# Optimization experiments

Hardware: AMD Instinct MI355X
Metric: run time of the kernel (lower is better)

## Reference

```python
import jax, jax.numpy as jnp
import numpy as np

B, T, C = 2, 2048, 1024
NH = 16
HD = C // NH

def build_alibi_bias(n_head, max_len):
    slopes = jnp.arange(1, n_head + 1, dtype=jnp.float32) / n_head  # [nh]
    ar = jnp.arange(max_len, dtype=jnp.float32)
    # bias[h, i, j] = slopes[h] * (j - i)
    return slopes[:, None, None] * (ar[None, None, :] - ar[None, :, None])

def setup_inputs() -> dict:
    key = jax.random.key(0)
    ks = jax.random.split(key, 7)
    s = 0.02
    return {
        "x": jax.random.normal(ks[0], (B, T, C), dtype=jnp.float32),
        "q_w": jax.random.normal(ks[1], (C, C), dtype=jnp.float32) * s,   # [in, out]
        "q_b": jnp.zeros((C,), dtype=jnp.float32),
        "kv_w": jax.random.normal(ks[2], (C, 2 * C), dtype=jnp.float32) * s,
        "kv_b": jnp.zeros((2 * C,), dtype=jnp.float32),
        "o_w": jax.random.normal(ks[3], (C, C), dtype=jnp.float32) * s,
        "o_b": jnp.zeros((C,), dtype=jnp.float32),
    }

def reference(x, q_w, q_b, kv_w, kv_b, o_w, o_b):
    Bx, Tx, Cx = x.shape
    q = (x @ q_w + q_b).reshape(Bx, Tx, NH, HD).transpose(0, 2, 1, 3)      # [B,nh,T,hd]
    kv = (x @ kv_w + kv_b).reshape(Bx, Tx, 2, NH, HD).transpose(2, 0, 3, 1, 4)
    k, v = kv[0], kv[1]                                                     # [B,nh,T,hd]
    att = jnp.einsum("bhqd,bhkd->bhqk", q, k) * (1.0 / np.sqrt(HD))        # [B,nh,T,T]
    att = att + build_alibi_bias(NH, Tx)[None]                              # ALiBi bias
    causal = jnp.tril(jnp.ones((Tx, Tx), dtype=bool))
    att = jnp.where(causal[None, None], att, -jnp.inf)
    att = jax.nn.softmax(att, axis=-1)
    y = jnp.einsum("bhqk,bhkd->bhqd", att, v)                               # [B,nh,T,hd]
    y = y.transpose(0, 2, 1, 3).reshape(Bx, Tx, Cx)
    return y @ o_w + o_b
```

## Files before the change

### kernel.cpp

```cpp
#include <hip/hip_runtime.h>
#include <hip/hip_bf16.h>

#define NB 2
#define NT 2048
#define NC 1024
#define NHD 16
#define HDD 64
#define LOG2E 1.4426950408889634f

typedef __attribute__((ext_vector_type(8))) short short8;
typedef __attribute__((ext_vector_type(4))) float f32x4;
typedef __attribute__((ext_vector_type(16))) float f32x16;

__device__ __forceinline__ ushort f2bf(float f) {
    union { float f; unsigned u; } v; v.f = f;
    unsigned u = v.u;
    unsigned r = (u + 0x7FFFu + ((u >> 16) & 1u)) >> 16;
    return (ushort)r;
}

__device__ __forceinline__ unsigned pkbf(float a, float b) {
    __hip_bfloat162 t = __float22bfloat162_rn(float2{a, b});
    unsigned u; __builtin_memcpy(&u, &t, 4); return u;
}

__device__ __forceinline__ void gload16(const ushort* g, ushort* l) {
    __builtin_amdgcn_global_load_lds((const __attribute__((address_space(1))) void*)g,
                                     (__attribute__((address_space(3))) void*)l, 16, 0, 0);
}

__device__ __forceinline__ void tcvt_tile(const float* __restrict__ src, ushort* __restrict__ dst,
                                          int Kd, int Nd, int kb, int nb)
{
    __shared__ ushort tile[64][68];
    const int tid = threadIdx.x;
    const int r = tid >> 2, c = (tid & 3) * 16;
    const float* sp = src + (size_t)(kb + r) * Nd + nb + c;
#pragma unroll
    for (int i = 0; i < 16; i += 4) {
        float4 v = *(const float4*)(sp + i);
        tile[r][c + i + 0] = f2bf(v.x);
        tile[r][c + i + 1] = f2bf(v.y);
        tile[r][c + i + 2] = f2bf(v.z);
        tile[r][c + i + 3] = f2bf(v.w);
    }
    __syncthreads();
    ushort* dp = dst + (size_t)(nb + r) * Kd + kb + c;
#pragma unroll
    for (int i = 0; i < 16; i += 8) {
        short8 o;
#pragma unroll
        for (int j = 0; j < 8; j++) o[j] = (short)tile[c + i + j][r];
        *(short8*)(dp + i) = o;
    }
}

__global__ __launch_bounds__(256)
void prep(const float* __restrict__ x, const float* __restrict__ q_w,
          const float* __restrict__ kv_w, const float* __restrict__ o_w,
          ushort* __restrict__ xb, ushort* __restrict__ wqkvT, ushort* __restrict__ woT)
{
    const int bid = blockIdx.x;
    if (bid < 2048) {
        int i = (bid * 256 + threadIdx.x) * 8;
        float4 a = *(const float4*)(x + i);
        float4 b = *(const float4*)(x + i + 4);
        short8 o;
        o[0] = (short)f2bf(a.x); o[1] = (short)f2bf(a.y);
        o[2] = (short)f2bf(a.z); o[3] = (short)f2bf(a.w);
        o[4] = (short)f2bf(b.x); o[5] = (short)f2bf(b.y);
        o[6] = (short)f2bf(b.z); o[7] = (short)f2bf(b.w);
        *(short8*)(xb + i) = o;
    } else if (bid < 2304) {
        int r = bid - 2048;
        tcvt_tile(q_w, wqkvT, 1024, 1024, (r & 15) * 64, (r >> 4) * 64);
    } else if (bid < 2816) {
        int r = bid - 2304;
        tcvt_tile(kv_w, wqkvT + 1024 * 1024, 1024, 2048, (r & 15) * 64, (r >> 4) * 64);
    } else {
        int r = bid - 2816;
        tcvt_tile(o_w, woT, 1024, 1024, (r & 15) * 64, (r >> 4) * 64);
    }
}

__global__ __launch_bounds__(256)
void vtr(const ushort* __restrict__ src, ushort* __restrict__ dst)
{
    __shared__ ushort tile[64][66];
    const int tid = threadIdx.x;
    const int bh = blockIdx.y;
    const int t0 = blockIdx.x * 64;
    const int r = tid >> 2, c = (tid & 3) * 16;
    const ushort* sp = src + ((size_t)bh * NT + t0 + r) * HDD + c;
    *(short8*)&tile[r][c]     = *(const short8*)sp;
    *(short8*)&tile[r][c + 8] = *(const short8*)(sp + 8);
    __syncthreads();
    ushort* dp = dst + ((size_t)bh * HDD + r) * NT + t0 + c;
    short8 o0, o1;
#pragma unroll
    for (int j = 0; j < 8; j++) { o0[j] = (short)tile[c + j][r]; o1[j] = (short)tile[c + 8 + j][r]; }
    *(short8*)dp = o0;
    *(short8*)(dp + 8) = o1;
}

template<int MODE>
__global__ __launch_bounds__(256)
void gemm128(const ushort* __restrict__ A, const ushort* __restrict__ Bt,
             const float* __restrict__ bias0, const float* __restrict__ bias1,
             ushort* __restrict__ Qo, ushort* __restrict__ Ko, ushort* __restrict__ Vo,
             float* __restrict__ Fo, int Kdim)
{
    __shared__ ushort Al[128 * 32];
    __shared__ ushort Bl[128 * 32];
    const int tid = threadIdx.x;
    const int lane = tid & 63, w = tid >> 6;
    const int wr = (w >> 1) * 64, wc = (w & 1) * 64;
    const int lg = lane >> 4, lc = lane & 15;
    const int bm = blockIdx.x * 128, bn = blockIdx.y * 128;

    f32x4 acc[4][4] = {};

    const int srow = lane >> 2, scol = (lane & 3) * 8;

    for (int k0 = 0; k0 < Kdim; k0 += 32) {
        __syncthreads();
#pragma unroll
        for (int c = 0; c < 2; c++) {
            int seg = w * 2 + c;
            int row = seg * 16 + srow;
            gload16(A  + (size_t)(bm + row) * Kdim + k0 + scol, &Al[seg * 512]);
            gload16(Bt + (size_t)(bn + row) * Kdim + k0 + scol, &Bl[seg * 512]);
        }
        __syncthreads();
        short8 af[4], bfv[4];
#pragma unroll
        for (int mt = 0; mt < 4; mt++) af[mt] = *(const short8*)&Al[(wr + mt*16 + lc) * 32 + lg*8];
#pragma unroll
        for (int nt = 0; nt < 4; nt++) bfv[nt] = *(const short8*)&Bl[(wc + nt*16 + lc) * 32 + lg*8];
#pragma unroll
        for (int mt = 0; mt < 4; mt++)
#pragma unroll
            for (int nt = 0; nt < 4; nt++)
                acc[mt][nt] = __builtin_amdgcn_mfma_f32_16x16x32_bf16(af[mt], bfv[nt], acc[mt][nt], 0, 0, 0);
    }

#pragma unroll
    for (int mt = 0; mt < 4; mt++) {
#pragma unroll
        for (int nt = 0; nt < 4; nt++) {
#pragma unroll
            for (int rr = 0; rr < 4; rr++) {
                int m = bm + wr + mt*16 + lg*4 + rr;
                int n = bn + wc + nt*16 + lc;
                float v = acc[mt][nt][rr];
                if (MODE == 0) {
                    int b = m >> 11, t = m & 2047;
                    if (n < NC) {
                        float q = (v + bias0[n]) * (0.125f * LOG2E);
                        int hh = n >> 6, d = n & 63;
                        Qo[(((size_t)b*NHD + hh)*NT + t)*HDD + d] = f2bf(q);
                    } else {
                        int j = n - NC;
                        float val = v + bias1[j];
                        int s = j >> 10;
                        int jj = j & 1023;
                        int hh = jj >> 6, d = jj & 63;
                        ushort* dst = s ? Vo : Ko;
                        dst[(((size_t)b*NHD + hh)*NT + t)*HDD + d] = f2bf(val);
                    }
                } else {
                    Fo[(size_t)m * NC + n] = v + bias0[n];
                }
            }
        }
    }
}

__global__ __launch_bounds__(128, 4)
void attn_fwd(const ushort* __restrict__ Q, const ushort* __restrict__ K,
              const ushort* __restrict__ Vt, ushort* __restrict__ Y)
{
    __shared__ ushort sb[4 * 64 * 72];
    const int tid = threadIdx.x;
    const int lane = tid & 63, w = tid >> 6;
    const int lo5 = lane & 31, hi = lane >> 5;
    const int qc = 31 - (int)(blockIdx.x >> 5);
    const int bh = blockIdx.x & 31;
    const int b = bh >> 4, h = bh & 15;

    const ushort* Qp = Q + (size_t)bh * NT * HDD;
    const ushort* Kp = K + (size_t)bh * NT * HDD;
    const ushort* Vp = Vt + (size_t)bh * HDD * NT;

    const int q0 = qc * 64 + w * 32;
    const int qlane = q0 + lo5;

    const float slope2 = (float)(h + 1) * (LOG2E / (float)NHD);

    short8 qf[4];
    {
        const ushort* qr = Qp + (size_t)qlane * HDD + 8 * hi;
#pragma unroll
        for (int kk = 0; kk < 4; kk++) qf[kk] = *(const short8*)(qr + kk * 16);
    }

    float bb[16];
#pragma unroll
    for (int r = 0; r < 16; r++) {
        int roff = (r & 3) + 8 * (r >> 2) + 4 * hi;
        bb[r] = slope2 * ((float)roff - (float)qlane);
    }

    float m_s = -1e30f, l_s = 0.f;
    f32x16 accO[2] = {};

    const int ntile = qc + 1;
    const int sr = tid >> 1, sd = (tid & 1) * 32;

    short8 pk[4], pv[4];
    {
        const ushort* kp = Kp + (size_t)sr * HDD + sd;
        const ushort* vp = Vp + (size_t)sr * NT + sd;
#pragma unroll
        for (int i = 0; i < 4; i++) {
            pk[i] = *(const short8*)(kp + i * 8);
            pv[i] = *(const short8*)(vp + i * 8);
        }
    }

    for (int t = 0; t < ntile; t++) {
        const int kv0 = t * 64;
        ushort* Kl = sb + (t & 1) * 2 * 64 * 72;
        ushort* Vl = Kl + 64 * 72;
#pragma unroll
        for (int i = 0; i < 4; i++) {
            *(short8*)&Kl[sr * 72 + sd + i * 8] = pk[i];
            *(short8*)&Vl[sr * 72 + sd + i * 8] = pv[i];
        }
        __syncthreads();

        if (t + 1 < ntile) {
            const int kv1 = kv0 + 64;
            const ushort* kp = Kp + (size_t)(kv1 + sr) * HDD + sd;
            const ushort* vp = Vp + (size_t)sr * NT + kv1 + sd;
#pragma unroll
            for (int i = 0; i < 4; i++) {
                pk[i] = *(const short8*)(kp + i * 8);
                pv[i] = *(const short8*)(vp + i * 8);
            }
        }

#pragma unroll
        for (int sub = 0; sub < 2; sub++) {
            const int kv0s = kv0 + sub * 32;
            if (kv0s > q0 + 31) continue;

            f32x16 S = {};
#pragma unroll
            for (int kk = 0; kk < 4; kk++) {
                short8 kf = *(const short8*)&Kl[(sub * 32 + lo5) * 72 + kk * 16 + 8 * hi];
                S = __builtin_amdgcn_mfma_f32_32x32x16_bf16(kf, qf[kk], S, 0, 0, 0);
            }

            const float sk = slope2 * (float)kv0s;
            float mloc = m_s - sk;

            if (kv0s + 31 > q0) {
#pragma unroll
                for (int r = 0; r < 16; r++) {
                    int kvr = kv0s + (r & 3) + 8 * (r >> 2) + 4 * hi;
                    S[r] = (kvr > qlane) ? -1e30f : (S[r] + bb[r]);
                }
            } else {
#pragma unroll
                for (int r = 0; r < 16; r++) S[r] = S[r] + bb[r];
            }

            float rmax = S[0];
#pragma unroll
            for (int r = 1; r < 16; r++) rmax = fmaxf(rmax, S[r]);
            rmax = fmaxf(rmax, __shfl_xor(rmax, 32));

            if (__any(rmax - mloc > 8.0f)) {
                float mn = fmaxf(mloc, rmax);
                float sc = __builtin_amdgcn_exp2f(mloc - mn);
                mloc = mn;
                l_s *= sc;
#pragma unroll
                for (int dt = 0; dt < 2; dt++)
#pragma unroll
                    for (int r = 0; r < 16; r++) accO[dt][r] *= sc;
            }
            m_s = mloc + sk;

            float p[16], sum = 0.f;
#pragma unroll
            for (int r = 0; r < 16; r++) {
                p[r] = __builtin_amdgcn_exp2f(S[r] - mloc);
                sum += p[r];
            }
            sum += __shfl_xor(sum, 32);
            l_s += sum;

            unsigned pw[8], px[8];
#pragma unroll
            for (int i = 0; i < 8; i++) pw[i] = pkbf(p[2 * i], p[2 * i + 1]);
#pragma unroll
            for (int i = 0; i < 8; i++) px[i] = __shfl_xor(pw[i], 32);
            union { unsigned u[4]; short8 s; } fa0, fa1;
            fa0.u[0] = hi ? px[2] : pw[0];
            fa0.u[1] = hi ? px[3] : pw[1];
            fa0.u[2] = hi ? pw[2] : px[0];
            fa0.u[3] = hi ? pw[3] : px[1];
            fa1.u[0] = hi ? px[6] : pw[4];
            fa1.u[1] = hi ? px[7] : pw[5];
            fa1.u[2] = hi ? pw[6] : px[4];
            fa1.u[3] = hi ? pw[7] : px[5];

#pragma unroll
            for (int dt = 0; dt < 2; dt++) {
                short8 vf0 = *(const short8*)&Vl[(dt * 32 + lo5) * 72 + sub * 32 + 8 * hi];
                short8 vf1 = *(const short8*)&Vl[(dt * 32 + lo5) * 72 + sub * 32 + 16 + 8 * hi];
                accO[dt] = __builtin_amdgcn_mfma_f32_32x32x16_bf16(vf0, fa0.s, accO[dt], 0, 0, 0);
                accO[dt] = __builtin_amdgcn_mfma_f32_32x32x16_bf16(vf1, fa1.s, accO[dt], 0, 0, 0);
            }
        }
    }

    const float invl = __builtin_amdgcn_rcpf(l_s);
    __syncthreads();
    ushort* myO = sb + w * 32 * 72;
#pragma unroll
    for (int dt = 0; dt < 2; dt++)
#pragma unroll
        for (int r = 0; r < 16; r++) {
            int d = dt * 32 + (r & 3) + 8 * (r >> 2) + 4 * hi;
            myO[lo5 * 72 + d] = f2bf(accO[dt][r] * invl);
        }
    __syncthreads();
    const int orow = lane >> 1, ocol = (lane & 1) * 32;
    const int qg = q0 + orow;
    ushort* yp = Y + ((size_t)b * NT + qg) * NC + h * HDD + ocol;
#pragma unroll
    for (int c = 0; c < 4; c++)
        *(short8*)(yp + c * 8) = *(const short8*)&myO[orow * 72 + ocol + c * 8];
}

extern "C" void kernel_launch(void* const* d_in, const int* in_sizes, int n_in,
                              void* d_out, int out_size, void* d_ws, size_t ws_size,
                              hipStream_t stream)
{
    const float* x    = (const float*)d_in[0];
    const float* q_w  = (const float*)d_in[1];
    const float* q_b  = (const float*)d_in[2];
    const float* kv_w = (const float*)d_in[3];
    const float* kv_b = (const float*)d_in[4];
    const float* o_w  = (const float*)d_in[5];
    const float* o_b  = (const float*)d_in[6];
    float* out = (float*)d_out;

    char* ws = (char*)d_ws;
    ushort* xb    = (ushort*)(ws);
    ushort* wqkvT = (ushort*)(ws + 8388608);
    ushort* woT   = (ushort*)(ws + 14680064);
    ushort* Qs    = (ushort*)(ws + 16777216);
    ushort* Ks    = (ushort*)(ws + 25165824);
    ushort* Vs    = (ushort*)(ws + 33554432);
    ushort* Ys    = (ushort*)(ws + 41943040);
    ushort* VsT   = xb;

    prep<<<3072, 256, 0, stream>>>(x, q_w, kv_w, o_w, xb, wqkvT, woT);
    gemm128<0><<<dim3(32,24), 256, 0, stream>>>(xb, wqkvT, q_b, kv_b, Qs, Ks, Vs, nullptr, 1024);
    vtr<<<dim3(32,32), 256, 0, stream>>>(Vs, VsT);
    attn_fwd<<<1024, 128, 0, stream>>>(Qs, Ks, VsT, Ys);
    gemm128<1><<<dim3(32,8), 256, 0, stream>>>(Ys, woT, o_b, nullptr, nullptr, nullptr, nullptr, out, 1024);
}
```

Measured before the change: 159.2 us.

## Split long causal attention rows across two blocks and merge with combine kernel

Attention blocks now cover 128 query rows with 4 waves instead of 64 rows with 2 waves. The key range of the 13 longest query tiles per head is split in half across two blocks, which write unnormalized partial outputs plus row max and sum into reused workspace. A new combine kernel merges these partials with log-sum-exp rescaling. The goal is to balance the causal workload across CUs. The change also drops LDS double buffering in favour of an extra barrier and adds s_setprio around the MFMA sections. The cost is an extra launch, bf16 rounding of the partials, and partial-result traffic through global memory.

```diff
diff --git a/kernel.cpp b/kernel.cpp
--- a/kernel.cpp
+++ b/kernel.cpp
@@ -17,6 +17,11 @@
     unsigned u = v.u;
     unsigned r = (u + 0x7FFFu + ((u >> 16) & 1u)) >> 16;
     return (ushort)r;
+}
+
+__device__ __forceinline__ float bf2f(ushort u) {
+    unsigned x = ((unsigned)u) << 16;
+    float f; __builtin_memcpy(&f, &x, 4); return f;
 }
 
 __device__ __forceinline__ unsigned pkbf(float a, float b) {
@@ -176,23 +181,42 @@
     }
 }
 
-__global__ __launch_bounds__(128, 4)
+__global__ __launch_bounds__(256, 3)
 void attn_fwd(const ushort* __restrict__ Q, const ushort* __restrict__ K,
-              const ushort* __restrict__ Vt, ushort* __restrict__ Y)
-{
-    __shared__ ushort sb[4 * 64 * 72];
+              const ushort* __restrict__ Vt, ushort* __restrict__ Y,
+              ushort* __restrict__ pool0, ushort* __restrict__ pool1,
+              float* __restrict__ mlb)
+{
+    __shared__ ushort sb[2 * 64 * 72];
+    ushort* Kl = sb;
+    ushort* Vl = sb + 64 * 72;
+
     const int tid = threadIdx.x;
     const int lane = tid & 63, w = tid >> 6;
     const int lo5 = lane & 31, hi = lane >> 5;
-    const int qc = 31 - (int)(blockIdx.x >> 5);
+    const int slot = (int)(blockIdx.x >> 5);
     const int bh = blockIdx.x & 31;
     const int b = bh >> 4, h = bh & 15;
+
+    int qt, t_begin, t_end, pi = 0;
+    const bool split = (slot < 26);
+    if (split) {
+        qt = 15 - (slot >> 1);
+        const int s = slot & 1;
+        t_begin = s * (qt + 1);
+        t_end = t_begin + (qt + 1);
+        pi = (bh * 13 + (qt - 3)) * 2 + s;
+    } else {
+        qt = 28 - slot;
+        t_begin = 0;
+        t_end = 2 * qt + 2;
+    }
 
     const ushort* Qp = Q + (size_t)bh * NT * HDD;
     const ushort* Kp = K + (size_t)bh * NT * HDD;
     const ushort* Vp = Vt + (size_t)bh * HDD * NT;
 
-    const int q0 = qc * 64 + w * 32;
+    const int q0 = qt * 128 + w * 32;
     const int qlane = q0 + lo5;
 
     const float slope2 = (float)(h + 1) * (LOG2E / (float)NHD);
@@ -214,40 +238,35 @@
     float m_s = -1e30f, l_s = 0.f;
     f32x16 accO[2] = {};
 
-    const int ntile = qc + 1;
-    const int sr = tid >> 1, sd = (tid & 1) * 32;
-
-    short8 pk[4], pv[4];
+    const int sr = tid >> 2, sd = (tid & 3) * 16;
+
+    short8 pk0, pk1, pv0, pv1;
     {
-        const ushort* kp = Kp + (size_t)sr * HDD + sd;
-        const ushort* vp = Vp + (size_t)sr * NT + sd;
-#pragma unroll
-        for (int i = 0; i < 4; i++) {
-            pk[i] = *(const short8*)(kp + i * 8);
-            pv[i] = *(const short8*)(vp + i * 8);
-        }
-    }
-
-    for (int t = 0; t < ntile; t++) {
+        const ushort* kp = Kp + (size_t)(t_begin * 64 + sr) * HDD + sd;
+        pk0 = *(const short8*)kp;
+        pk1 = *(const short8*)(kp + 8);
+        const ushort* vp = Vp + (size_t)sr * NT + t_begin * 64 + sd;
+        pv0 = *(const short8*)vp;
+        pv1 = *(const short8*)(vp + 8);
+    }
+
+    for (int t = t_begin; t < t_end; t++) {
         const int kv0 = t * 64;
-        ushort* Kl = sb + (t & 1) * 2 * 64 * 72;
-        ushort* Vl = Kl + 64 * 72;
-#pragma unroll
-        for (int i = 0; i < 4; i++) {
-            *(short8*)&Kl[sr * 72 + sd + i * 8] = pk[i];
-            *(short8*)&Vl[sr * 72 + sd + i * 8] = pv[i];
-        }
         __syncthreads();
-
-        if (t + 1 < ntile) {
+        *(short8*)&Kl[sr * 72 + sd]     = pk0;
+        *(short8*)&Kl[sr * 72 + sd + 8] = pk1;
+        *(short8*)&Vl[sr * 72 + sd]     = pv0;
+        *(short8*)&Vl[sr * 72 + sd + 8] = pv1;
+        __syncthreads();
+
+        if (t + 1 < t_end) {
             const int kv1 = kv0 + 64;
             const ushort* kp = Kp + (size_t)(kv1 + sr) * HDD + sd;
+            pk0 = *(const short8*)kp;
+            pk1 = *(const short8*)(kp + 8);
             const ushort* vp = Vp + (size_t)sr * NT + kv1 + sd;
-#pragma unroll
-            for (int i = 0; i < 4; i++) {
-                pk[i] = *(const short8*)(kp + i * 8);
-                pv[i] = *(const short8*)(vp + i * 8);
-            }
+            pv0 = *(const short8*)vp;
+            pv1 = *(const short8*)(vp + 8);
         }
 
 #pragma unroll
@@ -256,11 +275,13 @@
             if (kv0s > q0 + 31) continue;
 
             f32x16 S = {};
+            __builtin_amdgcn_s_setprio(1);
 #pragma unroll
             for (int kk = 0; kk < 4; kk++) {
                 short8 kf = *(const short8*)&Kl[(sub * 32 + lo5) * 72 + kk * 16 + 8 * hi];
                 S = __builtin_amdgcn_mfma_f32_32x32x16_bf16(kf, qf[kk], S, 0, 0, 0);
             }
+            __builtin_amdgcn_s_setprio(0);
 
             const float sk = slope2 * (float)kv0s;
             float mloc = m_s - sk;
@@ -317,6 +338,7 @@
             fa1.u[2] = hi ? pw[6] : px[4];
             fa1.u[3] = hi ? pw[7] : px[5];
 
+            __builtin_amdgcn_s_setprio(1);
 #pragma unroll
             for (int dt = 0; dt < 2; dt++) {
                 short8 vf0 = *(const short8*)&Vl[(dt * 32 + lo5) * 72 + sub * 32 + 8 * hi];
@@ -324,10 +346,11 @@
                 accO[dt] = __builtin_amdgcn_mfma_f32_32x32x16_bf16(vf0, fa0.s, accO[dt], 0, 0, 0);
                 accO[dt] = __builtin_amdgcn_mfma_f32_32x32x16_bf16(vf1, fa1.s, accO[dt], 0, 0, 0);
             }
-        }
-    }
-
-    const float invl = __builtin_amdgcn_rcpf(l_s);
+            __builtin_amdgcn_s_setprio(0);
+        }
+    }
+
+    const float invl = split ? 1.0f : __builtin_amdgcn_rcpf(l_s);
     __syncthreads();
     ushort* myO = sb + w * 32 * 72;
 #pragma unroll
@@ -337,13 +360,63 @@
             int d = dt * 32 + (r & 3) + 8 * (r >> 2) + 4 * hi;
             myO[lo5 * 72 + d] = f2bf(accO[dt][r] * invl);
         }
+    if (split && hi == 0) {
+        int rowin = w * 32 + lo5;
+        mlb[pi * 256 + rowin] = m_s;
+        mlb[pi * 256 + 128 + rowin] = l_s;
+    }
     __syncthreads();
     const int orow = lane >> 1, ocol = (lane & 1) * 32;
-    const int qg = q0 + orow;
-    ushort* yp = Y + ((size_t)b * NT + qg) * NC + h * HDD + ocol;
-#pragma unroll
-    for (int c = 0; c < 4; c++)
-        *(short8*)(yp + c * 8) = *(const short8*)&myO[orow * 72 + ocol + c * 8];
+    if (split) {
+        ushort* pp = (pi < 512 ? pool0 + (size_t)pi * 8192 : pool1 + (size_t)(pi - 512) * 8192)
+                     + (w * 32 + orow) * 64 + ocol;
+#pragma unroll
+        for (int c = 0; c < 4; c++)
+            *(short8*)(pp + c * 8) = *(const short8*)&myO[orow * 72 + ocol + c * 8];
+    } else {
+        ushort* yp = Y + ((size_t)b * NT + q0 + orow) * NC + h * HDD + ocol;
+#pragma unroll
+        for (int c = 0; c < 4; c++)
+            *(short8*)(yp + c * 8) = *(const short8*)&myO[orow * 72 + ocol + c * 8];
+    }
+}
+
+__global__ __launch_bounds__(256)
+void combine(const ushort* __restrict__ pool0, const ushort* __restrict__ pool1,
+             const float* __restrict__ mlb, ushort* __restrict__ Y)
+{
+    const int cb = blockIdx.x;
+    const int bh = cb / 13, qs = cb % 13;
+    const int qt = qs + 3;
+    const int b = bh >> 4, h = bh & 15;
+    const int pi0 = (bh * 13 + qs) * 2, pi1 = pi0 + 1;
+
+    const int tid = threadIdx.x;
+    const int r = tid >> 1, c0 = (tid & 1) * 32;
+
+    const float m0 = mlb[pi0 * 256 + r], l0 = mlb[pi0 * 256 + 128 + r];
+    const float m1 = mlb[pi1 * 256 + r], l1 = mlb[pi1 * 256 + 128 + r];
+    const float M = fmaxf(m0, m1);
+    const float a0 = __builtin_amdgcn_exp2f(m0 - M);
+    const float a1 = __builtin_amdgcn_exp2f(m1 - M);
+    const float inv = __builtin_amdgcn_rcpf(a0 * l0 + a1 * l1);
+
+    const ushort* p0 = (pi0 < 512 ? pool0 + (size_t)pi0 * 8192 : pool1 + (size_t)(pi0 - 512) * 8192) + r * 64 + c0;
+    const ushort* p1 = (pi1 < 512 ? pool0 + (size_t)pi1 * 8192 : pool1 + (size_t)(pi1 - 512) * 8192) + r * 64 + c0;
+    ushort* yp = Y + ((size_t)b * NT + qt * 128 + r) * NC + h * HDD + c0;
+
+#pragma unroll
+    for (int c = 0; c < 4; c++) {
+        short8 u0 = *(const short8*)(p0 + c * 8);
+        short8 u1 = *(const short8*)(p1 + c * 8);
+        short8 o;
+#pragma unroll
+        for (int j = 0; j < 8; j++) {
+            float v = (a0 * bf2f((ushort)u0[j]) + a1 * bf2f((ushort)u1[j])) * inv;
+            o[j] = (short)f2bf(v);
+        }
+        *(short8*)(yp + c * 8) = o;
+    }
 }
 
 extern "C" void kernel_launch(void* const* d_in, const int* in_sizes, int n_in,
@@ -368,10 +441,14 @@
     ushort* Vs    = (ushort*)(ws + 33554432);
     ushort* Ys    = (ushort*)(ws + 41943040);
     ushort* VsT   = xb;
+    ushort* pool0 = Vs;
+    ushort* pool1 = wqkvT;
+    float*  mlb   = (float*)(ws + 8388608 + 5242880);
 
     prep<<<3072, 256, 0, stream>>>(x, q_w, kv_w, o_w, xb, wqkvT, woT);
     gemm128<0><<<dim3(32,24), 256, 0, stream>>>(xb, wqkvT, q_b, kv_b, Qs, Ks, Vs, nullptr, 1024);
     vtr<<<dim3(32,32), 256, 0, stream>>>(Vs, VsT);
-    attn_fwd<<<1024, 128, 0, stream>>>(Qs, Ks, VsT, Ys);
+    attn_fwd<<<928, 256, 0, stream>>>(Qs, Ks, VsT, Ys, pool0, pool1, mlb);
+    combine<<<416, 256, 0, stream>>>(pool0, pool1, mlb, Ys);
     gemm128<1><<<dim3(32,8), 256, 0, stream>>>(Ys, woT, o_b, nullptr, nullptr, nullptr, nullptr, out, 1024);
 }
```

New measurement: 142.1 us. 10.7% less time.
